# Optimization experiments

Measured on AMD Instinct MI355X. Metric: run time of the kernel, lower is better.

Reference implementation:

```python
import jax, jax.numpy as jnp
import numpy as np

NV, NA, T, FD, C, E = 192, 64, 128, 1024, 128, 262144
SPK = 3
N = (NV + NA) * T  # 32768 total graph nodes
NEG = -1e30


def _seg_max(msg, dst, mask):
    # masked scatter-max; PyG fills segments with no messages with 0
    m = jnp.where(mask[:, None], msg, NEG)
    out = jax.ops.segment_max(m, dst, num_segments=N)
    return jnp.where(out > NEG * 0.5, out, 0.0)


def _edge_conv(x, src, dst, mask, W1, b1, W2, b2):
    # EdgeConv: max_j MLP(cat[x_i, x_j - x_i])
    xi = x[dst]
    h = jnp.concatenate([xi, x[src] - xi], axis=-1)  # [E, 2C]
    h = jax.nn.relu(h @ W1 + b1) @ W2 + b2
    return _seg_max(h, dst, mask)


def _sage_conv(x, src, dst, mask, Wl, bl, Wr):
    # SAGEConv: lin_l(mean_j x_j) + lin_r(x_i), lin_r has no bias
    mf = mask.astype(x.dtype)
    s = jax.ops.segment_sum(x[src] * mf[:, None], dst, num_segments=N)
    cnt = jax.ops.segment_sum(mf, dst, num_segments=N)
    mean = s / jnp.maximum(cnt, 1.0)[:, None]
    return mean @ Wl + bl + x @ Wr


def setup_inputs():
    ks = jax.random.split(jax.random.key(0), 24)
    s = 0.05
    vals = jnp.array([-3, -2, -1, 0, 1, 3], jnp.int32)
    return {
        "x_visual": jax.random.normal(ks[0], (NV, T, FD), jnp.float32),
        "x_audio": jax.random.normal(ks[1], (NA, T, FD), jnp.float32),
        "W011": jax.random.normal(ks[2], (FD, C)) * s, "b011": jnp.zeros((C,)),
        "W012": jax.random.normal(ks[3], (FD, C)) * s, "b012": jnp.zeros((C,)),
        "ecA_W1": jax.random.normal(ks[4], (2 * C, C)) * s, "ecA_b1": jnp.zeros((C,)),
        "ecA_W2": jax.random.normal(ks[5], (C, C)) * s, "ecA_b2": jnp.zeros((C,)),
        "ec1_W1": jax.random.normal(ks[6], (2 * C, C)) * s, "ec1_b1": jnp.zeros((C,)),
        "ec1_W2": jax.random.normal(ks[7], (C, C)) * s, "ec1_b2": jnp.zeros((C,)),
        "ec2_W1": jax.random.normal(ks[8], (2 * C, C)) * s, "ec2_b1": jnp.zeros((C,)),
        "ec2_W2": jax.random.normal(ks[9], (C, C)) * s, "ec2_b2": jnp.zeros((C,)),
        "ec3_W1": jax.random.normal(ks[10], (2 * C, C)) * s, "ec3_b1": jnp.zeros((C,)),
        "ec3_W2": jax.random.normal(ks[11], (C, C)) * s, "ec3_b2": jnp.zeros((C,)),
        "sage_Wl": jax.random.normal(ks[12], (C, C)) * s, "sage_bl": jnp.zeros((C,)),
        "sage_Wr": jax.random.normal(ks[13], (C, C)) * s,
        "fc_W": jax.random.normal(ks[14], (C, 1)) * s, "fc_b": jnp.zeros((1,)),
        "edge_index": jax.random.randint(ks[15], (2, E), 0, N, dtype=jnp.int32),
        "edge_attr": vals[jax.random.randint(ks[16], (E,), 0, 6)],
        "speakers": SPK,
    }


def reference(x_visual, x_audio, W011, b011, W012, b012,
              ecA_W1, ecA_b1, ecA_W2, ecA_b2,
              ec1_W1, ec1_b1, ec1_W2, ec1_b2,
              ec2_W1, ec2_b1, ec2_W2, ec2_b2,
              ec3_W1, ec3_b1, ec3_W2, ec3_b2,
              sage_Wl, sage_bl, sage_Wr, fc_W, fc_b,
              edge_index, edge_attr, speakers):
    xv = x_visual @ W011 + b011          # [NV, T, C]
    xa = x_audio @ W012 + b012           # [NA, T, C]
    x = jnp.concatenate([xv, xa], axis=0).reshape(-1, C)  # [N, C]
    src, dst = edge_index[0], edge_index[1]
    m_audio = edge_attr == -2
    m_vpa = edge_attr == -3
    m_acv = edge_attr == 3
    m1 = (edge_attr >= 0) & (edge_attr <= 1)
    m2 = (edge_attr <= 0) & (edge_attr >= -1)
    m3 = jnp.abs(edge_attr) <= 1
    # Visual_Add_Audio_GNN: max-aggregate (x_i + x_j)
    xa_g = jax.nn.relu(_seg_max(x[dst] + x[src], dst, m_vpa))
    a = jax.nn.relu(_edge_conv(xa_g, src, dst, m_audio, ecA_W1, ecA_b1, ecA_W2, ecA_b2))
    a_res = a @ fc_W + fc_b              # [N, 1] per-node audio scores
    # Audio_Weight_Add_Visual_GNN: sum-aggregate (w_j * x_j + x_i)
    wmsg = jnp.where(m_acv[:, None], a_res[src] * x[src] + x[dst], 0.0)
    xv2 = jax.nn.relu(jax.ops.segment_sum(wmsg, dst, num_segments=N))

    def branch(mask, W1, b1, W2, b2):
        h = jax.nn.relu(_edge_conv(xv2, src, dst, mask, W1, b1, W2, b2))
        return jax.nn.relu(_sage_conv(h, src, dst, mask, sage_Wl, sage_bl, sage_Wr))

    xo = (branch(m1, ec1_W1, ec1_b1, ec1_W2, ec1_b2)
          + branch(m2, ec2_W1, ec2_b1, ec2_W2, ec2_b2)
          + branch(m3, ec3_W1, ec3_b1, ec3_W2, ec3_b2))
    # gather main-speaker visual nodes
    idx = (jnp.arange(0, NV * T, speakers * T)[:, None] + jnp.arange(T)).reshape(-1)
    return xo[idx]
```

## Files before the change

kernel.cpp:

```cpp
#include <hip/hip_runtime.h>
#include <cstdint>
#include <cstddef>

#define NVv 192
#define NAa 64
#define TT 128
#define FDd 1024
#define CCc 128
#define EEe 262144
#define NNn 32768

typedef _Float16 f16x8 __attribute__((ext_vector_type(8)));
typedef float f32x4 __attribute__((ext_vector_type(4)));

#define CAP0 65536
#define CAP1 65536
#define CAP2 65536
#define CAP3 98304
#define CAP4 98304
#define CAP5 147456
#define ARENA_TOTAL (CAP0+CAP1+CAP2+CAP3+CAP4+CAP5)

__device__ __forceinline__ void eval_masks(int a, bool m[6]) {
    m[0] = (a == -3); m[1] = (a == -2); m[2] = (a == 3);
    m[3] = (a >= 0) & (a <= 1);
    m[4] = (a >= -1) & (a <= 0);
    m[5] = (a >= -1) & (a <= 1);
}

__global__ __launch_bounds__(256) void k_zero(float* __restrict__ p) {
    size_t i = (size_t)blockIdx.x * 1024 + (size_t)threadIdx.x * 4;
    *(float4*)(p + i) = make_float4(0.f, 0.f, 0.f, 0.f);
}

__global__ __launch_bounds__(256) void k_zero4(
    const int* __restrict__ hist, const int* __restrict__ base,
    float* __restrict__ AH0, float* __restrict__ AH1,
    float* __restrict__ AH2, float* __restrict__ AH3)
{
    int col = threadIdx.x & 127, sub = threadIdx.x >> 7;
    const int js[4] = {1, 3, 4, 5};
    float* AHs[4] = {AH0, AH1, AH2, AH3};
    for (int d = blockIdx.x * 2 + sub; d < NNn; d += gridDim.x * 2) {
#pragma unroll
        for (int jj = 0; jj < 4; ++jj) {
            int j = js[jj];
            int c = hist[j * NNn + d];
            bool need;
            if (c == 0) need = true;
            else {
                int b = base[j * NNn + d], e = b + c;
                need = ((b & 63) == 0) || ((e & 63) == 0) || ((b >> 6) != ((e - 1) >> 6));
            }
            if (need) AHs[jj][(size_t)d * 128 + col] = 0.f;
        }
    }
}

__global__ __launch_bounds__(256) void k_wprep_big(
    const float* __restrict__ W011, const float* __restrict__ W012,
    _Float16* __restrict__ dst)
{
    int idx = blockIdx.x * 256 + threadIdx.x;
    int which = idx >> 17;
    int r = idx & 131071;
    int n = r >> 10, k = r & 1023;
    const float* src = which ? W012 : W011;
    dst[idx] = (_Float16)src[k * 128 + n];
}

struct WSmall { const float* p[14]; };

__global__ __launch_bounds__(256) void k_wprep_small(WSmall ws, _Float16* __restrict__ dst)
{
    int idx = blockIdx.x * 256 + threadIdx.x;
    int seg = idx >> 14;
    int r = idx & 16383;
    int n = r >> 7, k = r & 127;
    const float* src = ws.p[seg];
    float v = src[k * 128 + n];
    if (seg < 12 && (seg % 3) == 0) v -= src[16384 + k * 128 + n];
    dst[idx] = (_Float16)v;
}

__global__ __launch_bounds__(256) void k_hist(
    const int* __restrict__ attr, const int* __restrict__ edst,
    int* __restrict__ hist)
{
    int e = blockIdx.x * 256 + threadIdx.x;
    int a = attr[e], d = edst[e];
    bool m[6]; eval_masks(a, m);
#pragma unroll
    for (int j = 0; j < 6; ++j)
        if (m[j]) atomicAdd(&hist[j * NNn + d], 1);
}

__global__ __launch_bounds__(256) void k_scan_a(
    const int* __restrict__ hist, int* __restrict__ base, int* __restrict__ bsum)
{
    __shared__ int wsum[4];
    int bid = blockIdx.x;
    int idx = bid * 256 + threadIdx.x;
    int tid = threadIdx.x, lane = tid & 63, wv = tid >> 6;
    int v = hist[idx];
    int x = v;
#pragma unroll
    for (int off = 1; off < 64; off <<= 1) {
        int y = __shfl_up(x, off, 64);
        if (lane >= off) x += y;
    }
    if (lane == 63) wsum[wv] = x;
    __syncthreads();
    int add = 0;
    for (int w = 0; w < wv; ++w) add += wsum[w];
    base[idx] = add + x - v;
    if (tid == 255) bsum[bid] = add + x;
}

__global__ __launch_bounds__(384) void k_scan_b(int* __restrict__ bsum, int* __restrict__ cnts)
{
    int wv = threadIdx.x >> 6;
    int lane = threadIdx.x & 63;
    int run = 0;
#pragma unroll
    for (int c0 = 0; c0 < 128; c0 += 64) {
        int v = bsum[wv * 128 + c0 + lane];
        int x = v;
#pragma unroll
        for (int off = 1; off < 64; off <<= 1) {
            int y = __shfl_up(x, off, 64);
            if (lane >= off) x += y;
        }
        bsum[wv * 128 + c0 + lane] = run + (x - v);
        run += __shfl(x, 63, 64);
    }
    if (lane == 0) cnts[wv] = run;
}

__global__ __launch_bounds__(256) void k_scan_c(int* __restrict__ base, const int* __restrict__ bsum)
{
    base[blockIdx.x * 256 + threadIdx.x] += bsum[blockIdx.x];
}

__global__ __launch_bounds__(256) void k_fill(
    const int* __restrict__ esrc, const int* __restrict__ edst,
    const int* __restrict__ attr, const int* __restrict__ base,
    int* __restrict__ fill, int2* __restrict__ arena)
{
    int e = blockIdx.x * 256 + threadIdx.x;
    int a = attr[e];
    int s = esrc[e], d = edst[e];
    bool m[6]; eval_masks(a, m);
    const int caps[6] = {CAP0, CAP1, CAP2, CAP3, CAP4, CAP5};
    const int offs[6] = {0, CAP0, CAP0+CAP1, CAP0+CAP1+CAP2,
                         CAP0+CAP1+CAP2+CAP3, CAP0+CAP1+CAP2+CAP3+CAP4};
#pragma unroll
    for (int j = 0; j < 6; ++j) {
        if (m[j]) {
            int pos = base[j * NNn + d] + atomicAdd(&fill[j * NNn + d], 1);
            if (pos < caps[j]) arena[offs[j] + pos] = make_int2(s, d);
        }
    }
}

__global__ __launch_bounds__(512) void k_proj(
    const float* __restrict__ xv, const float* __restrict__ xa,
    const _Float16* __restrict__ BTv, const _Float16* __restrict__ BTa,
    float* __restrict__ Pp0, float* __restrict__ Pp1)
{
    __shared__ _Float16 Bl[2][128][136];
    const int tid = threadIdx.x, wave = tid >> 6, lane = tid & 63;
    const int tile = blockIdx.x >> 1, kh = blockIdx.x & 1;
    const float* A; const _Float16* BT; int mbase, obase;
    if (tile < 192) { A = xv; BT = BTv; mbase = tile * 128; obase = mbase; }
    else { A = xa; BT = BTa; mbase = (tile - 192) * 128; obase = 24576 + mbase; }
    float* Pout = kh ? Pp1 : Pp0;
    const int kbase = kh * 512;

    const int mrow = mbase + wave * 16 + (lane & 15);
    const int fk   = (lane >> 4) * 8;
    f32x4 acc[8];
#pragma unroll
    for (int i = 0; i < 8; ++i) acc[i] = (f32x4){0,0,0,0};

#pragma unroll
    for (int it = 0; it < 4; ++it) {
        int c = it * 512 + tid;
        int n = c >> 4, koff = (c & 15) * 8;
        *(f16x8*)&Bl[0][n][koff] = *(const f16x8*)(BT + (size_t)n * 1024 + kbase + koff);
    }
    f16x8 af[4];
#pragma unroll
    for (int t4 = 0; t4 < 4; ++t4) {
        const float* asrc = A + (size_t)mrow * 1024 + kbase + t4 * 32 + fk;
        float4 a0 = *(const float4*)asrc;
        float4 a1 = *(const float4*)(asrc + 4);
        af[t4] = (f16x8){ (_Float16)a0.x, (_Float16)a0.y, (_Float16)a0.z, (_Float16)a0.w,
                          (_Float16)a1.x, (_Float16)a1.y, (_Float16)a1.z, (_Float16)a1.w };
    }
    __syncthreads();

    for (int kc = 0; kc < 4; ++kc) {
        const int cur = kc & 1;
        f16x8 nf[4];
        if (kc < 3) {
            const int nxt = cur ^ 1;
#pragma unroll
            for (int it = 0; it < 4; ++it) {
                int c = it * 512 + tid;
                int n = c >> 4, koff = (c & 15) * 8;
                *(f16x8*)&Bl[nxt][n][koff] =
                    *(const f16x8*)(BT + (size_t)n * 1024 + kbase + (kc + 1) * 128 + koff);
            }
#pragma unroll
            for (int t4 = 0; t4 < 4; ++t4) {
                const float* asrc = A + (size_t)mrow * 1024 + kbase + (kc + 1) * 128 + t4 * 32 + fk;
                float4 a0 = *(const float4*)asrc;
                float4 a1 = *(const float4*)(asrc + 4);
                nf[t4] = (f16x8){ (_Float16)a0.x, (_Float16)a0.y, (_Float16)a0.z, (_Float16)a0.w,
                                  (_Float16)a1.x, (_Float16)a1.y, (_Float16)a1.z, (_Float16)a1.w };
            }
        }
#pragma unroll
        for (int t4 = 0; t4 < 4; ++t4)
#pragma unroll
            for (int nt = 0; nt < 8; ++nt) {
                f16x8 bf = *(const f16x8*)&Bl[cur][nt * 16 + (lane & 15)][t4 * 32 + fk];
                acc[nt] = __builtin_amdgcn_mfma_f32_16x16x32_f16(af[t4], bf, acc[nt], 0, 0, 0);
            }
        if (kc < 3) {
#pragma unroll
            for (int t4 = 0; t4 < 4; ++t4) af[t4] = nf[t4];
        }
        __syncthreads();
    }
    const int cbase = lane & 15, rloc = (lane >> 4) * 4;
    const int wgrp = wave & 3;
    float* Hsf = (float*)&Bl[0][0][0] + (size_t)wgrp * 16 * 132;
#pragma unroll
    for (int grp = 0; grp < 2; ++grp) {
        if ((wave >> 2) == grp) {
#pragma unroll
            for (int nt = 0; nt < 8; ++nt) {
                int c2 = nt * 16 + cbase;
#pragma unroll
                for (int rr = 0; rr < 4; ++rr)
                    Hsf[(rloc + rr) * 132 + c2] = acc[nt][rr];
            }
#pragma unroll
            for (int it = 0; it < 8; ++it) {
                int id = it * 64 + lane;
                int row = id >> 5, off = (id & 31) * 4;
                float4 v = *(float4*)&Hsf[row * 132 + off];
                *(float4*)&Pout[(size_t)(obase + wave * 16 + row) * 128 + off] = v;
            }
        }
        __syncthreads();
    }
}

__global__ __launch_bounds__(256) void k_reduce(
    const float* __restrict__ Pp0, const float* __restrict__ Pp1,
    const float* __restrict__ b011, const float* __restrict__ b012,
    float* __restrict__ X)
{
    size_t f = (size_t)blockIdx.x * 256 + threadIdx.x;
    size_t i = f * 4;
    int col = (int)(i & 127);
    int row = (int)(i >> 7);
    const float* bias = (row < 24576) ? b011 : b012;
    float4 a = *(const float4*)(Pp0 + i);
    float4 b = *(const float4*)(Pp1 + i);
    float4 bb = *(const float4*)(bias + col);
    float4 o = make_float4(a.x + b.x + bb.x, a.y + b.y + bb.y,
                           a.z + b.z + bb.z, a.w + b.w + bb.w);
    *(float4*)(X + i) = o;
}

__global__ __launch_bounds__(256) void k_pv(
    const float* __restrict__ A,
    const _Float16* __restrict__ BT1, const float* __restrict__ b1,
    const _Float16* __restrict__ BT2,
    _Float16* __restrict__ P, _Float16* __restrict__ V)
{
    __shared__ _Float16 Bl1[128][136];
    __shared__ _Float16 Bl2[128][136];
    __shared__ float bb[128];
    const int tid = threadIdx.x, wave = tid >> 6, lane = tid & 63;
    const int r0 = blockIdx.x * 64 + wave * 16;

    const int fk = (lane >> 4) * 8;
    const int mrow = blockIdx.x * 64 + wave * 16 + (lane & 15);
    float4 a0[4], a1[4];
#pragma unroll
    for (int t4 = 0; t4 < 4; ++t4) {
        const float* asrc = A + (size_t)mrow * 128 + t4 * 32 + fk;
        a0[t4] = *(const float4*)asrc;
        a1[t4] = *(const float4*)(asrc + 4);
    }
#pragma unroll
    for (int it = 0; it < 8; ++it) {
        int c = it * 256 + tid;
        int n = c >> 4, koff = (c & 15) * 8;
        *(f16x8*)&Bl1[n][koff] = *(const f16x8*)(BT1 + (size_t)n * 128 + koff);
        *(f16x8*)&Bl2[n][koff] = *(const f16x8*)(BT2 + (size_t)n * 128 + koff);
    }
    if (tid < 128) bb[tid] = b1[tid];
    __syncthreads();

    f16x8 af[4];
#pragma unroll
    for (int t4 = 0; t4 < 4; ++t4)
        af[t4] = (f16x8){ (_Float16)a0[t4].x, (_Float16)a0[t4].y, (_Float16)a0[t4].z, (_Float16)a0[t4].w,
                          (_Float16)a1[t4].x, (_Float16)a1[t4].y, (_Float16)a1[t4].z, (_Float16)a1[t4].w };
    f32x4 acc1[8], acc2[8];
#pragma unroll
    for (int i = 0; i < 8; ++i) { acc1[i] = (f32x4){0,0,0,0}; acc2[i] = (f32x4){0,0,0,0}; }
#pragma unroll
    for (int t4 = 0; t4 < 4; ++t4)
#pragma unroll
        for (int nt = 0; nt < 8; ++nt) {
            f16x8 bf1 = *(const f16x8*)&Bl1[nt * 16 + (lane & 15)][t4 * 32 + fk];
            f16x8 bf2 = *(const f16x8*)&Bl2[nt * 16 + (lane & 15)][t4 * 32 + fk];
            acc1[nt] = __builtin_amdgcn_mfma_f32_16x16x32_f16(af[t4], bf1, acc1[nt], 0, 0, 0);
            acc2[nt] = __builtin_amdgcn_mfma_f32_16x16x32_f16(af[t4], bf2, acc2[nt], 0, 0, 0);
        }
    __syncthreads();
    _Float16* Hs = &Bl1[0][0] + (size_t)wave * 16 * 136;
    const int cbase = lane & 15, rloc = (lane >> 4) * 4;
#pragma unroll
    for (int nt = 0; nt < 8; ++nt) {
        int c2 = nt * 16 + cbase;
        float bvv = bb[c2];
#pragma unroll
        for (int rr = 0; rr < 4; ++rr)
            Hs[(rloc + rr) * 136 + c2] = (_Float16)(acc1[nt][rr] + bvv);
    }
#pragma unroll
    for (int it = 0; it < 4; ++it) {
        int id = it * 64 + lane;
        int row = id >> 4, koff = (id & 15) * 8;
        *(f16x8*)&P[(size_t)(r0 + row) * 128 + koff] = *(f16x8*)&Hs[row * 136 + koff];
    }
#pragma unroll
    for (int nt = 0; nt < 8; ++nt) {
        int c2 = nt * 16 + cbase;
#pragma unroll
        for (int rr = 0; rr < 4; ++rr)
            Hs[(rloc + rr) * 136 + c2] = (_Float16)acc2[nt][rr];
    }
#pragma unroll
    for (int it = 0; it < 4; ++it) {
        int id = it * 64 + lane;
        int row = id >> 4, koff = (id & 15) * 8;
        *(f16x8*)&V[(size_t)(r0 + row) * 128 + koff] = *(f16x8*)&Hs[row * 136 + koff];
    }
}

__global__ __launch_bounds__(256, 3) void k_edge_mlp(
    const _Float16* __restrict__ P, const _Float16* __restrict__ V,
    const _Float16* __restrict__ W2T, const float* __restrict__ b2,
    const int2* __restrict__ list, const int* __restrict__ cntp, int cap,
    float* __restrict__ agg)
{
    __shared__ _Float16 Rl[64][136];
    __shared__ _Float16 W2l[128][136];
    __shared__ float b2l[128];
    __shared__ int2 eSD[64];
    __shared__ unsigned char gstart[66];
    __shared__ int gdst[64];
    __shared__ int ngrS;

    int cnt = min(*cntp, cap);
    int ntiles = (cnt + 63) >> 6;
    if ((int)blockIdx.x >= ntiles) return;

    const int tid  = threadIdx.x;
    const int wave = tid >> 6;
    const int lane = tid & 63;

#pragma unroll
    for (int i = 0; i < 8; ++i) {
        int c = tid + i * 256;
        int n = c >> 4, koff = (c & 15) * 8;
        *(f16x8*)&W2l[n][koff] = *(const f16x8*)(W2T + n * 128 + koff);
    }
    if (tid < 128) b2l[tid] = b2[tid];

    const int col   = tid & 127;
    const int half  = tid >> 7;
    const int frow  = wave * 16 + (lane & 15);
    const int fq    = (lane >> 4) * 8;
    const int rbase = wave * 16 + (lane >> 4) * 4;
    const int cbase = lane & 15;
    const int rrow  = tid >> 4;
    const int rch   = (tid & 15) * 8;

    for (int t = blockIdx.x; t < ntiles; t += gridDim.x) {
        __syncthreads();
        if (tid < 64) {
            int e = t * 64 + tid;
            eSD[tid] = (e < cnt) ? list[e] : make_int2(0, -1);
        }
        __syncthreads();
        if (tid < 64) {
            int d = eSD[tid].y;
            bool flag = (tid == 0) || (d != eSD[tid - 1].y);
            unsigned long long bm = __ballot(flag);
            int rank = (int)__popcll(bm & ((1ull << tid) - 1ull));
            if (flag) { gstart[rank] = (unsigned char)tid; gdst[rank] = d; }
            if (tid == 0) {
                int ng = (int)__popcll(bm);
                ngrS = ng;
                gstart[ng] = 64;
            }
        }
#pragma unroll
        for (int p = 0; p < 4; ++p) {
            int i = p * 16 + rrow;
            int2 sd = eSD[i];
            f16x8 rv = {0, 0, 0, 0, 0, 0, 0, 0};
            if (sd.y >= 0) {
                f16x8 pv = *(const f16x8*)(P + (size_t)sd.y * 128 + rch);
                f16x8 vv = *(const f16x8*)(V + (size_t)sd.x * 128 + rch);
                rv = pv + vv;
#pragma unroll
                for (int q = 0; q < 8; ++q)
                    rv[q] = (rv[q] > (_Float16)0.f) ? rv[q] : (_Float16)0.f;
            }
            *(f16x8*)&Rl[i][rch] = rv;
        }
        __syncthreads();

        f32x4 acc[8];
#pragma unroll
        for (int i = 0; i < 8; ++i) acc[i] = (f32x4){0,0,0,0};
#pragma unroll
        for (int t4 = 0; t4 < 4; ++t4) {
            f16x8 af = *(const f16x8*)&Rl[frow][t4 * 32 + fq];
#pragma unroll
            for (int nt = 0; nt < 8; ++nt) {
                f16x8 bf = *(const f16x8*)&W2l[nt * 16 + (lane & 15)][t4 * 32 + fq];
                acc[nt] = __builtin_amdgcn_mfma_f32_16x16x32_f16(af, bf, acc[nt], 0, 0, 0);
            }
        }
        __syncthreads();
#pragma unroll
        for (int nt = 0; nt < 8; ++nt) {
            int c2 = nt * 16 + cbase;
            float bv = b2l[c2];
#pragma unroll
            for (int rr = 0; rr < 4; ++rr)
                Rl[rbase + rr][c2] = (_Float16)fmaxf(acc[nt][rr] + bv, 0.f);
        }
        __syncthreads();
        int ng = ngrS;
        for (int g = half; g < ng; g += 2) {
            int s = gstart[g], e = gstart[g + 1];
            int d = gdst[g];
            if (d < 0) continue;
            float m = 0.f;
            for (int i = s; i < e; ++i)
                m = fmaxf(m, (float)Rl[i][col]);
            size_t o = (size_t)d * 128 + col;
            if (s == 0 || e == 64)
                atomicMax((unsigned int*)&agg[o], __float_as_uint(m));
            else
                agg[o] = m;
        }
    }
}

__global__ __launch_bounds__(256) void k_csr_vpa(
    const float* __restrict__ X, const int2* __restrict__ list,
    const int* __restrict__ base, const int* __restrict__ cntarr, int cap,
    float* __restrict__ S)
{
    int col = threadIdx.x & 127;
    int sub = threadIdx.x >> 7;
    for (int d = blockIdx.x * 2 + sub; d < NNn; d += gridDim.x * 2) {
        int c = cntarr[d];
        float v = 0.f;
        if (c > 0) {
            int b = base[d];
            int end = min(b + c, cap);
            float mx = -3.0e38f;
            for (int i = b; i < end; ++i)
                mx = fmaxf(mx, X[(size_t)list[i].x * 128 + col]);
            v = fmaxf(X[(size_t)d * 128 + col] + mx, 0.f);
        }
        S[(size_t)d * 128 + col] = v;
    }
}

__global__ __launch_bounds__(256) void k_csr_acv(
    const float* __restrict__ X, const float* __restrict__ ares,
    const int2* __restrict__ list,
    const int* __restrict__ base, const int* __restrict__ cntarr, int cap,
    float* __restrict__ S)
{
    int col = threadIdx.x & 127;
    int sub = threadIdx.x >> 7;
    for (int d = blockIdx.x * 2 + sub; d < NNn; d += gridDim.x * 2) {
        int c = cntarr[d];
        float v = 0.f;
        if (c > 0) {
            int b = base[d];
            int end = min(b + c, cap);
            float s = 0.f;
            for (int i = b; i < end; ++i) {
                int sr = list[i].x;
                s += ares[sr] * X[(size_t)sr * 128 + col];
            }
            v = fmaxf(s + (float)c * X[(size_t)d * 128 + col], 0.f);
        }
        S[(size_t)d * 128 + col] = v;
    }
}

__global__ __launch_bounds__(256) void k_csr_meanc(
    const float* __restrict__ AH, const int2* __restrict__ list,
    const int* __restrict__ basej, const int* __restrict__ histj, int cap,
    const int* __restrict__ spk, int ntarg,
    float* __restrict__ S1c, float* __restrict__ AHc)
{
    int col = threadIdx.x & 127;
    int sub = threadIdx.x >> 7;
    int step = spk[0] * TT;
    for (int ci = blockIdx.x * 2 + sub; ci < ntarg; ci += gridDim.x * 2) {
        int d = (ci >> 7) * step + (ci & 127);
        int c = histj[d];
        float v = 0.f;
        if (c > 0) {
            int b = basej[d];
            int end = min(b + c, cap);
            float s = 0.f;
            for (int i = b; i < end; ++i)
                s += AH[(size_t)list[i].x * 128 + col];
            v = s / (float)c;
        }
        S1c[(size_t)ci * 128 + col] = v;
        AHc[(size_t)ci * 128 + col] = AH[(size_t)d * 128 + col];
    }
}

__global__ __launch_bounds__(256) void k_fc(
    const float* __restrict__ A, const float* __restrict__ W,
    const float* __restrict__ b, float* __restrict__ ares)
{
    int node = blockIdx.x * 4 + (threadIdx.x >> 6);
    int lane = threadIdx.x & 63;
    const float* row = A + (size_t)node * 128;
    float v = row[lane] * W[lane] + row[lane + 64] * W[lane + 64];
#pragma unroll
    for (int off = 32; off > 0; off >>= 1) v += __shfl_down(v, off, 64);
    if (lane == 0) ares[node] = v + b[0];
}

__global__ __launch_bounds__(256) void k_sage_out(
    const float* __restrict__ S1c, const float* __restrict__ AHc,
    const _Float16* __restrict__ WlT, const _Float16* __restrict__ WrT,
    const float* __restrict__ bl, float* __restrict__ out, int ntarg)
{
    __shared__ _Float16 Al[64][40];
    __shared__ _Float16 Bl[128][40];
    const int tid  = threadIdx.x;
    const int wave = tid >> 6;
    const int lane = tid & 63;
    const int m0   = blockIdx.x * 64;

    f32x4 accB[8], accO[8];
#pragma unroll
    for (int i = 0; i < 8; ++i) { accB[i] = (f32x4){0,0,0,0}; accO[i] = (f32x4){0,0,0,0}; }

    const int ar = tid >> 2;
    const int ak = (tid & 3) * 8;
    const int fr = wave * 16 + (lane & 15);
    const int fk = (lane >> 4) * 8;
    const int rbase = wave * 16 + (lane >> 4) * 4;
    const int cbase = lane & 15;

    for (int seg = 0; seg < 6; ++seg) {
        int b = seg >> 1, which = seg & 1;
        const float* A = (which ? AHc : S1c) + (size_t)b * ntarg * 128;
        const _Float16* BT = which ? WrT : WlT;
        for (int k0 = 0; k0 < 128; k0 += 32) {
            __syncthreads();
            const float* asrc = A + (size_t)(m0 + ar) * 128 + (k0 + ak);
            float4 a0 = *(const float4*)asrc;
            float4 a1 = *(const float4*)(asrc + 4);
            f16x8 av = { (_Float16)a0.x, (_Float16)a0.y, (_Float16)a0.z, (_Float16)a0.w,
                         (_Float16)a1.x, (_Float16)a1.y, (_Float16)a1.z, (_Float16)a1.w };
            *(f16x8*)&Al[ar][ak] = av;
#pragma unroll
            for (int i = 0; i < 2; ++i) {
                int c = tid + i * 256;
                int n = c >> 2, koff = (c & 3) * 8;
                *(f16x8*)&Bl[n][koff] = *(const f16x8*)(BT + (size_t)n * 128 + k0 + koff);
            }
            __syncthreads();
            f16x8 af = *(const f16x8*)&Al[fr][fk];
#pragma unroll
            for (int nt = 0; nt < 8; ++nt) {
                f16x8 bf = *(const f16x8*)&Bl[nt * 16 + (lane & 15)][fk];
                accB[nt] = __builtin_amdgcn_mfma_f32_16x16x32_f16(af, bf, accB[nt], 0, 0, 0);
            }
        }
        if (which) {
#pragma unroll
            for (int nt = 0; nt < 8; ++nt) {
                int col = nt * 16 + cbase;
                float bv = bl[col];
#pragma unroll
                for (int rr = 0; rr < 4; ++rr) {
                    accO[nt][rr] += fmaxf(accB[nt][rr] + bv, 0.f);
                    accB[nt][rr] = 0.f;
                }
            }
        }
    }
#pragma unroll
    for (int nt = 0; nt < 8; ++nt) {
        int col = nt * 16 + cbase;
#pragma unroll
        for (int rr = 0; rr < 4; ++rr)
            out[(size_t)(m0 + rbase + rr) * 128 + col] = accO[nt][rr];
    }
}

extern "C" void kernel_launch(void* const* d_in, const int* in_sizes, int n_in,
                              void* d_out, int out_size, void* d_ws, size_t ws_size,
                              hipStream_t stream)
{
    (void)in_sizes; (void)n_in; (void)ws_size;
    const float* xv   = (const float*)d_in[0];
    const float* xa   = (const float*)d_in[1];
    const float* W011 = (const float*)d_in[2];
    const float* b011 = (const float*)d_in[3];
    const float* W012 = (const float*)d_in[4];
    const float* b012 = (const float*)d_in[5];
    const float* ecW1[4] = {(const float*)d_in[6],  (const float*)d_in[10],
                            (const float*)d_in[14], (const float*)d_in[18]};
    const float* ecb1[4] = {(const float*)d_in[7],  (const float*)d_in[11],
                            (const float*)d_in[15], (const float*)d_in[19]};
    const float* ecW2[4] = {(const float*)d_in[8],  (const float*)d_in[12],
                            (const float*)d_in[16], (const float*)d_in[20]};
    const float* ecb2[4] = {(const float*)d_in[9],  (const float*)d_in[13],
                            (const float*)d_in[17], (const float*)d_in[21]};
    const float* sageWl = (const float*)d_in[22];
    const float* sagebl = (const float*)d_in[23];
    const float* sageWr = (const float*)d_in[24];
    const float* fcW    = (const float*)d_in[25];
    const float* fcb    = (const float*)d_in[26];
    const int*   esrc   = (const int*)d_in[27];
    const int*   edst   = esrc + EEe;
    const int*   attr   = (const int*)d_in[28];
    const int*   spk    = (const int*)d_in[29];
    float* out = (float*)d_out;
    const int ntarg = out_size >> 7;

    const size_t NC = (size_t)NNn * CCc;
    float* ws   = (float*)d_ws;
    float* X    = ws;
    float* S1   = ws + 1 * NC;
    float* XV2  = ws + 2 * NC;
    float* AHc  = ws + 3 * NC;
    float* AH0  = ws + 4 * NC;
    float* AH1  = ws + 5 * NC;
    float* AH2  = ws + 6 * NC;
    float* AH3  = ws + 7 * NC;
    _Float16* P16 = (_Float16*)(ws + 8 * NC);
    _Float16* V16 = P16 + NC;
    float* ARES = ws + 9 * NC;
    int*   cnts = (int*)(ARES + NNn);
    int*   bsum = cnts + 16;
    int*   hist = bsum + 1024;
    int*   fill = hist + 6 * NNn;
    int*   base = fill + 6 * NNn;
    int2*  arena = (int2*)(base + 6 * NNn);
    _Float16* WT = (_Float16*)(arena + ARENA_TOTAL);
    float* AHb[4] = {AH0, AH1, AH2, AH3};

    const int offs[6] = {0, CAP0, CAP0+CAP1, CAP0+CAP1+CAP2,
                         CAP0+CAP1+CAP2+CAP3, CAP0+CAP1+CAP2+CAP3+CAP4};
    const int caps[6] = {CAP0, CAP1, CAP2, CAP3, CAP4, CAP5};

    const _Float16* W011T = WT;
    const _Float16* W012T = WT + 131072;
    const _Float16* WTs   = WT + 262144;
    const _Float16* WlT   = WTs + 12 * 16384;
    const _Float16* WrT   = WTs + 13 * 16384;

    k_wprep_big<<<1024, 256, 0, stream>>>(W011, W012, WT);
    WSmall wsm;
    for (int i = 0; i < 4; ++i) {
        wsm.p[3*i + 0] = ecW1[i];
        wsm.p[3*i + 1] = ecW1[i] + 16384;
        wsm.p[3*i + 2] = ecW2[i];
    }
    wsm.p[12] = sageWl; wsm.p[13] = sageWr;
    k_wprep_small<<<896, 256, 0, stream>>>(wsm, (_Float16*)WTs);
    k_zero<<<(2 * 6 * NNn) / 1024, 256, 0, stream>>>((float*)hist);
    k_hist<<<EEe / 256, 256, 0, stream>>>(attr, edst, hist);
    k_scan_a<<<768, 256, 0, stream>>>(hist, base, bsum);
    k_scan_b<<<1, 384, 0, stream>>>(bsum, cnts);
    k_scan_c<<<768, 256, 0, stream>>>(base, bsum);
    k_fill<<<EEe / 256, 256, 0, stream>>>(esrc, edst, attr, base, fill, arena);
    k_zero4<<<2048, 256, 0, stream>>>(hist, base, AH0, AH1, AH2, AH3);

    k_proj<<<512, 512, 0, stream>>>(xv, xa, W011T, W012T, S1, XV2);
    k_reduce<<<(int)(NC / 1024), 256, 0, stream>>>(S1, XV2, b011, b012, X);
    k_csr_vpa<<<2048, 256, 0, stream>>>(X, arena + offs[0], base + 0 * NNn,
                                        hist + 0 * NNn, caps[0], S1);
    k_pv<<<512, 256, 0, stream>>>(S1, WTs, ecb1[0], WTs + 16384, P16, V16);
    k_edge_mlp<<<2048, 256, 0, stream>>>(P16, V16, WTs + 2 * 16384, ecb2[0],
                                         arena + offs[1], cnts + 1, caps[1], AH0);
    k_fc<<<NNn / 4, 256, 0, stream>>>(AH0, fcW, fcb, ARES);
    k_csr_acv<<<2048, 256, 0, stream>>>(X, ARES, arena + offs[2], base + 2 * NNn,
                                        hist + 2 * NNn, caps[2], XV2);
    for (int b = 0; b < 3; ++b) {
        int j = 3 + b;
        const _Float16* Wd = WTs + (3 * (b + 1)) * 16384;
        k_pv<<<512, 256, 0, stream>>>(XV2, Wd, ecb1[b + 1], Wd + 16384, P16, V16);
        k_edge_mlp<<<2048, 256, 0, stream>>>(P16, V16, Wd + 2 * 16384, ecb2[b + 1],
                                             arena + offs[j], cnts + j, caps[j], AHb[b + 1]);
        k_csr_meanc<<<2048, 256, 0, stream>>>(AHb[b + 1], arena + offs[j], base + j * NNn,
                                              hist + j * NNn, caps[j], spk, ntarg,
                                              S1 + (size_t)b * ntarg * 128,
                                              AHc + (size_t)b * ntarg * 128);
    }
    k_sage_out<<<ntarg / 64, 256, 0, stream>>>(S1, AHc, WlT, WrT, sagebl, out, ntarg);
}
```

Baseline: 554.4 us.

## Batch three branch passes into single launches and merge setup kernels

Merges the weight prep and histogram zeroing into one setup kernel, and the CSR fill and AH zeroing into one kernel. The three branch EdgeConv stages (P/V projection, edge MLP, mean aggregation) now each run as one launch covering all three branches. Separate P/V buffers are carved out of dead workspace regions (X, AHc) so the branches can run side by side. This cuts launch count and serial dependencies and gives the GPU more work per launch, at the cost of buffer aliasing risk and a one-tile-per-block edge MLP grid of 5376 blocks.

```diff
diff --git a/kernel.cpp b/kernel.cpp
--- a/kernel.cpp
+++ b/kernel.cpp
@@ -20,6 +20,12 @@
 #define CAP4 98304
 #define CAP5 147456
 #define ARENA_TOTAL (CAP0+CAP1+CAP2+CAP3+CAP4+CAP5)
+#define OFF0 0
+#define OFF1 CAP0
+#define OFF2 (CAP0+CAP1)
+#define OFF3 (CAP0+CAP1+CAP2)
+#define OFF4 (CAP0+CAP1+CAP2+CAP3)
+#define OFF5 (CAP0+CAP1+CAP2+CAP3+CAP4)
 
 __device__ __forceinline__ void eval_masks(int a, bool m[6]) {
     m[0] = (a == -3); m[1] = (a == -2); m[2] = (a == 3);
@@ -28,59 +34,38 @@
     m[5] = (a >= -1) & (a <= 1);
 }
 
-__global__ __launch_bounds__(256) void k_zero(float* __restrict__ p) {
-    size_t i = (size_t)blockIdx.x * 1024 + (size_t)threadIdx.x * 4;
-    *(float4*)(p + i) = make_float4(0.f, 0.f, 0.f, 0.f);
-}
-
-__global__ __launch_bounds__(256) void k_zero4(
-    const int* __restrict__ hist, const int* __restrict__ base,
-    float* __restrict__ AH0, float* __restrict__ AH1,
-    float* __restrict__ AH2, float* __restrict__ AH3)
-{
-    int col = threadIdx.x & 127, sub = threadIdx.x >> 7;
-    const int js[4] = {1, 3, 4, 5};
-    float* AHs[4] = {AH0, AH1, AH2, AH3};
-    for (int d = blockIdx.x * 2 + sub; d < NNn; d += gridDim.x * 2) {
-#pragma unroll
-        for (int jj = 0; jj < 4; ++jj) {
-            int j = js[jj];
-            int c = hist[j * NNn + d];
-            bool need;
-            if (c == 0) need = true;
-            else {
-                int b = base[j * NNn + d], e = b + c;
-                need = ((b & 63) == 0) || ((e & 63) == 0) || ((b >> 6) != ((e - 1) >> 6));
-            }
-            if (need) AHs[jj][(size_t)d * 128 + col] = 0.f;
-        }
-    }
-}
-
-__global__ __launch_bounds__(256) void k_wprep_big(
+struct WSmall { const float* p[14]; };
+struct PV3  { const _Float16* Wd[3]; const _Float16* Wv[3]; const float* b1[3];
+              _Float16* P[3]; _Float16* V[3]; };
+struct MLP3 { const _Float16* W2[3]; const float* b2[3];
+              const _Float16* P[3]; const _Float16* V[3]; float* AH[3]; };
+
+__global__ __launch_bounds__(256) void k_setup(
     const float* __restrict__ W011, const float* __restrict__ W012,
-    _Float16* __restrict__ dst)
-{
-    int idx = blockIdx.x * 256 + threadIdx.x;
-    int which = idx >> 17;
-    int r = idx & 131071;
-    int n = r >> 10, k = r & 1023;
-    const float* src = which ? W012 : W011;
-    dst[idx] = (_Float16)src[k * 128 + n];
-}
-
-struct WSmall { const float* p[14]; };
-
-__global__ __launch_bounds__(256) void k_wprep_small(WSmall ws, _Float16* __restrict__ dst)
-{
-    int idx = blockIdx.x * 256 + threadIdx.x;
-    int seg = idx >> 14;
-    int r = idx & 16383;
-    int n = r >> 7, k = r & 127;
-    const float* src = ws.p[seg];
-    float v = src[k * 128 + n];
-    if (seg < 12 && (seg % 3) == 0) v -= src[16384 + k * 128 + n];
-    dst[idx] = (_Float16)v;
+    WSmall wsm, _Float16* __restrict__ WT, _Float16* __restrict__ WTs,
+    float* __restrict__ hf)
+{
+    int blk = blockIdx.x, tid = threadIdx.x;
+    if (blk < 1024) {
+        int idx = blk * 256 + tid;
+        int which = idx >> 17;
+        int r = idx & 131071;
+        int n = r >> 10, k = r & 1023;
+        const float* src = which ? W012 : W011;
+        WT[idx] = (_Float16)src[k * 128 + n];
+    } else if (blk < 1920) {
+        int idx = (blk - 1024) * 256 + tid;
+        int seg = idx >> 14;
+        int r = idx & 16383;
+        int n = r >> 7, k = r & 127;
+        const float* src = wsm.p[seg];
+        float v = src[k * 128 + n];
+        if (seg < 12 && (seg % 3) == 0) v -= src[16384 + k * 128 + n];
+        WTs[idx] = (_Float16)v;
+    } else {
+        size_t i = (size_t)(blk - 1920) * 1024 + (size_t)tid * 4;
+        *(float4*)(hf + i) = make_float4(0.f, 0.f, 0.f, 0.f);
+    }
 }
 
 __global__ __launch_bounds__(256) void k_hist(
@@ -99,8 +84,7 @@
     const int* __restrict__ hist, int* __restrict__ base, int* __restrict__ bsum)
 {
     __shared__ int wsum[4];
-    int bid = blockIdx.x;
-    int idx = bid * 256 + threadIdx.x;
+    int idx = blockIdx.x * 256 + threadIdx.x;
     int tid = threadIdx.x, lane = tid & 63, wv = tid >> 6;
     int v = hist[idx];
     int x = v;
@@ -114,7 +98,7 @@
     int add = 0;
     for (int w = 0; w < wv; ++w) add += wsum[w];
     base[idx] = add + x - v;
-    if (tid == 255) bsum[bid] = add + x;
+    if (tid == 255) bsum[blockIdx.x] = add + x;
 }
 
 __global__ __launch_bounds__(384) void k_scan_b(int* __restrict__ bsum, int* __restrict__ cnts)
@@ -142,23 +126,46 @@
     base[blockIdx.x * 256 + threadIdx.x] += bsum[blockIdx.x];
 }
 
-__global__ __launch_bounds__(256) void k_fill(
+__global__ __launch_bounds__(256) void k_fill_zero(
     const int* __restrict__ esrc, const int* __restrict__ edst,
     const int* __restrict__ attr, const int* __restrict__ base,
-    int* __restrict__ fill, int2* __restrict__ arena)
-{
-    int e = blockIdx.x * 256 + threadIdx.x;
-    int a = attr[e];
-    int s = esrc[e], d = edst[e];
-    bool m[6]; eval_masks(a, m);
-    const int caps[6] = {CAP0, CAP1, CAP2, CAP3, CAP4, CAP5};
-    const int offs[6] = {0, CAP0, CAP0+CAP1, CAP0+CAP1+CAP2,
-                         CAP0+CAP1+CAP2+CAP3, CAP0+CAP1+CAP2+CAP3+CAP4};
-#pragma unroll
-    for (int j = 0; j < 6; ++j) {
-        if (m[j]) {
-            int pos = base[j * NNn + d] + atomicAdd(&fill[j * NNn + d], 1);
-            if (pos < caps[j]) arena[offs[j] + pos] = make_int2(s, d);
+    int* __restrict__ fill, int2* __restrict__ arena, const int* __restrict__ hist,
+    float* __restrict__ AH0, float* __restrict__ AH1,
+    float* __restrict__ AH2, float* __restrict__ AH3)
+{
+    int blk = blockIdx.x, tid = threadIdx.x;
+    if (blk < 1024) {
+        int e = blk * 256 + tid;
+        int a = attr[e];
+        int s = esrc[e], d = edst[e];
+        bool m[6]; eval_masks(a, m);
+        const int caps[6] = {CAP0, CAP1, CAP2, CAP3, CAP4, CAP5};
+        const int offs[6] = {OFF0, OFF1, OFF2, OFF3, OFF4, OFF5};
+#pragma unroll
+        for (int j = 0; j < 6; ++j) {
+            if (m[j]) {
+                int pos = base[j * NNn + d] + atomicAdd(&fill[j * NNn + d], 1);
+                if (pos < caps[j]) arena[offs[j] + pos] = make_int2(s, d);
+            }
+        }
+    } else {
+        int zb = blk - 1024;
+        int col = tid & 127, sub = tid >> 7;
+        const int js[4] = {1, 3, 4, 5};
+        float* AHs[4] = {AH0, AH1, AH2, AH3};
+        for (int d = zb * 2 + sub; d < NNn; d += 2048 * 2) {
+#pragma unroll
+            for (int jj = 0; jj < 4; ++jj) {
+                int j = js[jj];
+                int c = hist[j * NNn + d];
+                bool need;
+                if (c == 0) need = true;
+                else {
+                    int b = base[j * NNn + d], e = b + c;
+                    need = ((b & 63) == 0) || ((e & 63) == 0) || ((b >> 6) != ((e - 1) >> 6));
+                }
+                if (need) AHs[jj][(size_t)d * 128 + col] = 0.f;
+            }
         }
     }
 }
@@ -272,25 +279,20 @@
     float4 a = *(const float4*)(Pp0 + i);
     float4 b = *(const float4*)(Pp1 + i);
     float4 bb = *(const float4*)(bias + col);
-    float4 o = make_float4(a.x + b.x + bb.x, a.y + b.y + bb.y,
-                           a.z + b.z + bb.z, a.w + b.w + bb.w);
-    *(float4*)(X + i) = o;
-}
-
-__global__ __launch_bounds__(256) void k_pv(
-    const float* __restrict__ A,
-    const _Float16* __restrict__ BT1, const float* __restrict__ b1,
-    const _Float16* __restrict__ BT2,
-    _Float16* __restrict__ P, _Float16* __restrict__ V)
-{
-    __shared__ _Float16 Bl1[128][136];
-    __shared__ _Float16 Bl2[128][136];
-    __shared__ float bb[128];
+    *(float4*)(X + i) = make_float4(a.x + b.x + bb.x, a.y + b.y + bb.y,
+                                    a.z + b.z + bb.z, a.w + b.w + bb.w);
+}
+
+__device__ __forceinline__ void pv_body(
+    const float* __restrict__ A, const _Float16* __restrict__ BT1,
+    const float* __restrict__ b1, const _Float16* __restrict__ BT2,
+    _Float16* __restrict__ P, _Float16* __restrict__ V, int tileblk,
+    _Float16 (*Bl1)[136], _Float16 (*Bl2)[136], float* bb)
+{
     const int tid = threadIdx.x, wave = tid >> 6, lane = tid & 63;
-    const int r0 = blockIdx.x * 64 + wave * 16;
-
+    const int r0 = tileblk * 64 + wave * 16;
     const int fk = (lane >> 4) * 8;
-    const int mrow = blockIdx.x * 64 + wave * 16 + (lane & 15);
+    const int mrow = r0 + (lane & 15);
     float4 a0[4], a1[4];
 #pragma unroll
     for (int t4 = 0; t4 < 4; ++t4) {
@@ -354,6 +356,123 @@
         int id = it * 64 + lane;
         int row = id >> 4, koff = (id & 15) * 8;
         *(f16x8*)&V[(size_t)(r0 + row) * 128 + koff] = *(f16x8*)&Hs[row * 136 + koff];
+    }
+}
+
+__global__ __launch_bounds__(256) void k_pv(
+    const float* __restrict__ A, const _Float16* __restrict__ BT1,
+    const float* __restrict__ b1, const _Float16* __restrict__ BT2,
+    _Float16* __restrict__ P, _Float16* __restrict__ V)
+{
+    __shared__ _Float16 Bl1[128][136];
+    __shared__ _Float16 Bl2[128][136];
+    __shared__ float bb[128];
+    pv_body(A, BT1, b1, BT2, P, V, blockIdx.x, Bl1, Bl2, bb);
+}
+
+__global__ __launch_bounds__(256) void k_pv3(const float* __restrict__ A, PV3 p)
+{
+    __shared__ _Float16 Bl1[128][136];
+    __shared__ _Float16 Bl2[128][136];
+    __shared__ float bb[128];
+    int b = blockIdx.x >> 9, t = blockIdx.x & 511;
+    pv_body(A, p.Wd[b], p.b1[b], p.Wv[b], p.P[b], p.V[b], t, Bl1, Bl2, bb);
+}
+
+__device__ __forceinline__ void mlp_tile(
+    const _Float16* __restrict__ P, const _Float16* __restrict__ V,
+    const _Float16* __restrict__ W2T, const float* __restrict__ b2,
+    const int2* __restrict__ list, int cnt, int t, float* __restrict__ agg,
+    _Float16 (*Rl)[136], _Float16 (*W2l)[136], float* b2l,
+    int2* eSD, unsigned char* gstart, int* gdst, int* ngrS)
+{
+    const int tid  = threadIdx.x;
+    const int wave = tid >> 6;
+    const int lane = tid & 63;
+#pragma unroll
+    for (int i = 0; i < 8; ++i) {
+        int c = tid + i * 256;
+        int n = c >> 4, koff = (c & 15) * 8;
+        *(f16x8*)&W2l[n][koff] = *(const f16x8*)(W2T + n * 128 + koff);
+    }
+    if (tid < 128) b2l[tid] = b2[tid];
+    if (tid < 64) {
+        int e = t * 64 + tid;
+        eSD[tid] = (e < cnt) ? list[e] : make_int2(0, -1);
+    }
+    __syncthreads();
+    if (tid < 64) {
+        int d = eSD[tid].y;
+        bool flag = (tid == 0) || (d != eSD[tid - 1].y);
+        unsigned long long bm = __ballot(flag);
+        int rank = (int)__popcll(bm & ((1ull << tid) - 1ull));
+        if (flag) { gstart[rank] = (unsigned char)tid; gdst[rank] = d; }
+        if (tid == 0) {
+            int ng = (int)__popcll(bm);
+            *ngrS = ng;
+            gstart[ng] = 64;
+        }
+    }
+    const int rrow = tid >> 4;
+    const int rch  = (tid & 15) * 8;
+#pragma unroll
+    for (int p = 0; p < 4; ++p) {
+        int i = p * 16 + rrow;
+        int2 sd = eSD[i];
+        f16x8 rv = {0, 0, 0, 0, 0, 0, 0, 0};
+        if (sd.y >= 0) {
+            f16x8 pv = *(const f16x8*)(P + (size_t)sd.y * 128 + rch);
+            f16x8 vv = *(const f16x8*)(V + (size_t)sd.x * 128 + rch);
+            rv = pv + vv;
+#pragma unroll
+            for (int q = 0; q < 8; ++q)
+                rv[q] = (rv[q] > (_Float16)0.f) ? rv[q] : (_Float16)0.f;
+        }
+        *(f16x8*)&Rl[i][rch] = rv;
+    }
+    __syncthreads();
+
+    const int frow  = wave * 16 + (lane & 15);
+    const int fq    = (lane >> 4) * 8;
+    f32x4 acc[8];
+#pragma unroll
+    for (int i = 0; i < 8; ++i) acc[i] = (f32x4){0,0,0,0};
+#pragma unroll
+    for (int t4 = 0; t4 < 4; ++t4) {
+        f16x8 af = *(const f16x8*)&Rl[frow][t4 * 32 + fq];
+#pragma unroll
+        for (int nt = 0; nt < 8; ++nt) {
+            f16x8 bf = *(const f16x8*)&W2l[nt * 16 + (lane & 15)][t4 * 32 + fq];
+            acc[nt] = __builtin_amdgcn_mfma_f32_16x16x32_f16(af, bf, acc[nt], 0, 0, 0);
+        }
+    }
+    __syncthreads();
+    const int rbase = wave * 16 + (lane >> 4) * 4;
+    const int cbase = lane & 15;
+#pragma unroll
+    for (int nt = 0; nt < 8; ++nt) {
+        int c2 = nt * 16 + cbase;
+        float bv = b2l[c2];
+#pragma unroll
+        for (int rr = 0; rr < 4; ++rr)
+            Rl[rbase + rr][c2] = (_Float16)fmaxf(acc[nt][rr] + bv, 0.f);
+    }
+    __syncthreads();
+    const int col  = tid & 127;
+    const int half = tid >> 7;
+    int ng = *ngrS;
+    for (int g = half; g < ng; g += 2) {
+        int s = gstart[g], e = gstart[g + 1];
+        int d = gdst[g];
+        if (d < 0) continue;
+        float m = 0.f;
+        for (int i = s; i < e; ++i)
+            m = fmaxf(m, (float)Rl[i][col]);
+        size_t o = (size_t)d * 128 + col;
+        if (s == 0 || e == 64)
+            atomicMax((unsigned int*)&agg[o], __float_as_uint(m));
+        else
+            agg[o] = m;
     }
 }
 
@@ -370,105 +489,38 @@
     __shared__ unsigned char gstart[66];
     __shared__ int gdst[64];
     __shared__ int ngrS;
-
     int cnt = min(*cntp, cap);
     int ntiles = (cnt + 63) >> 6;
     if ((int)blockIdx.x >= ntiles) return;
-
-    const int tid  = threadIdx.x;
-    const int wave = tid >> 6;
-    const int lane = tid & 63;
-
-#pragma unroll
-    for (int i = 0; i < 8; ++i) {
-        int c = tid + i * 256;
-        int n = c >> 4, koff = (c & 15) * 8;
-        *(f16x8*)&W2l[n][koff] = *(const f16x8*)(W2T + n * 128 + koff);
-    }
-    if (tid < 128) b2l[tid] = b2[tid];
-
-    const int col   = tid & 127;
-    const int half  = tid >> 7;
-    const int frow  = wave * 16 + (lane & 15);
-    const int fq    = (lane >> 4) * 8;
-    const int rbase = wave * 16 + (lane >> 4) * 4;
-    const int cbase = lane & 15;
-    const int rrow  = tid >> 4;
-    const int rch   = (tid & 15) * 8;
-
     for (int t = blockIdx.x; t < ntiles; t += gridDim.x) {
-        __syncthreads();
-        if (tid < 64) {
-            int e = t * 64 + tid;
-            eSD[tid] = (e < cnt) ? list[e] : make_int2(0, -1);
-        }
-        __syncthreads();
-        if (tid < 64) {
-            int d = eSD[tid].y;
-            bool flag = (tid == 0) || (d != eSD[tid - 1].y);
-            unsigned long long bm = __ballot(flag);
-            int rank = (int)__popcll(bm & ((1ull << tid) - 1ull));
-            if (flag) { gstart[rank] = (unsigned char)tid; gdst[rank] = d; }
-            if (tid == 0) {
-                int ng = (int)__popcll(bm);
-                ngrS = ng;
-                gstart[ng] = 64;
-            }
-        }
-#pragma unroll
-        for (int p = 0; p < 4; ++p) {
-            int i = p * 16 + rrow;
-            int2 sd = eSD[i];
-            f16x8 rv = {0, 0, 0, 0, 0, 0, 0, 0};
-            if (sd.y >= 0) {
-                f16x8 pv = *(const f16x8*)(P + (size_t)sd.y * 128 + rch);
-                f16x8 vv = *(const f16x8*)(V + (size_t)sd.x * 128 + rch);
-                rv = pv + vv;
-#pragma unroll
-                for (int q = 0; q < 8; ++q)
-                    rv[q] = (rv[q] > (_Float16)0.f) ? rv[q] : (_Float16)0.f;
-            }
-            *(f16x8*)&Rl[i][rch] = rv;
-        }
-        __syncthreads();
-
-        f32x4 acc[8];
-#pragma unroll
-        for (int i = 0; i < 8; ++i) acc[i] = (f32x4){0,0,0,0};
-#pragma unroll
-        for (int t4 = 0; t4 < 4; ++t4) {
-            f16x8 af = *(const f16x8*)&Rl[frow][t4 * 32 + fq];
-#pragma unroll
-            for (int nt = 0; nt < 8; ++nt) {
-                f16x8 bf = *(const f16x8*)&W2l[nt * 16 + (lane & 15)][t4 * 32 + fq];
-                acc[nt] = __builtin_amdgcn_mfma_f32_16x16x32_f16(af, bf, acc[nt], 0, 0, 0);
-            }
-        }
-        __syncthreads();
-#pragma unroll
-        for (int nt = 0; nt < 8; ++nt) {
-            int c2 = nt * 16 + cbase;
-            float bv = b2l[c2];
-#pragma unroll
-            for (int rr = 0; rr < 4; ++rr)
-                Rl[rbase + rr][c2] = (_Float16)fmaxf(acc[nt][rr] + bv, 0.f);
-        }
-        __syncthreads();
-        int ng = ngrS;
-        for (int g = half; g < ng; g += 2) {
-            int s = gstart[g], e = gstart[g + 1];
-            int d = gdst[g];
-            if (d < 0) continue;
-            float m = 0.f;
-            for (int i = s; i < e; ++i)
-                m = fmaxf(m, (float)Rl[i][col]);
-            size_t o = (size_t)d * 128 + col;
-            if (s == 0 || e == 64)
-                atomicMax((unsigned int*)&agg[o], __float_as_uint(m));
-            else
-                agg[o] = m;
-        }
-    }
+        if (t != (int)blockIdx.x) __syncthreads();
+        mlp_tile(P, V, W2T, b2, list, cnt, t, agg,
+                 Rl, W2l, b2l, eSD, gstart, gdst, &ngrS);
+    }
+}
+
+__global__ __launch_bounds__(256, 3) void k_edge_mlp3(
+    MLP3 p, const int2* __restrict__ arena, const int* __restrict__ cnts)
+{
+    __shared__ _Float16 Rl[64][136];
+    __shared__ _Float16 W2l[128][136];
+    __shared__ float b2l[128];
+    __shared__ int2 eSD[64];
+    __shared__ unsigned char gstart[66];
+    __shared__ int gdst[64];
+    __shared__ int ngrS;
+    const int caps[3] = {CAP3, CAP4, CAP5};
+    const int offs[3] = {OFF3, OFF4, OFF5};
+    int c0 = min(cnts[3], CAP3), c1 = min(cnts[4], CAP4), c2 = min(cnts[5], CAP5);
+    int n0 = (c0 + 63) >> 6, n1 = (c1 + 63) >> 6, n2 = (c2 + 63) >> 6;
+    int t = blockIdx.x, b;
+    if (t < n0) b = 0;
+    else if (t < n0 + n1) { b = 1; t -= n0; }
+    else if (t < n0 + n1 + n2) { b = 2; t -= n0 + n1; }
+    else return;
+    int cnt = min(cnts[3 + b], caps[b]);
+    mlp_tile(p.P[b], p.V[b], p.W2[b], p.b2[b], arena + offs[b], cnt, t, p.AH[b],
+             Rl, W2l, b2l, eSD, gstart, gdst, &ngrS);
 }
 
 __global__ __launch_bounds__(256) void k_csr_vpa(
@@ -518,29 +570,39 @@
     }
 }
 
-__global__ __launch_bounds__(256) void k_csr_meanc(
-    const float* __restrict__ AH, const int2* __restrict__ list,
-    const int* __restrict__ basej, const int* __restrict__ histj, int cap,
+__global__ __launch_bounds__(256) void k_meanc3(
+    float* const AH1, float* const AH2, float* const AH3,
+    const int2* __restrict__ arena,
+    const int* __restrict__ base, const int* __restrict__ hist,
     const int* __restrict__ spk, int ntarg,
     float* __restrict__ S1c, float* __restrict__ AHc)
 {
     int col = threadIdx.x & 127;
     int sub = threadIdx.x >> 7;
     int step = spk[0] * TT;
-    for (int ci = blockIdx.x * 2 + sub; ci < ntarg; ci += gridDim.x * 2) {
+    const int caps[3] = {CAP3, CAP4, CAP5};
+    const int offs[3] = {OFF3, OFF4, OFF5};
+    const float* AHs[3] = {AH1, AH2, AH3};
+    int total = 3 * ntarg;
+    for (int ci2 = blockIdx.x * 2 + sub; ci2 < total; ci2 += gridDim.x * 2) {
+        int b = ci2 / ntarg;
+        int ci = ci2 - b * ntarg;
+        int j = 3 + b;
+        const float* AH = AHs[b];
+        const int2* list = arena + offs[b];
         int d = (ci >> 7) * step + (ci & 127);
-        int c = histj[d];
+        int c = hist[j * NNn + d];
         float v = 0.f;
         if (c > 0) {
-            int b = basej[d];
-            int end = min(b + c, cap);
+            int bs = base[j * NNn + d];
+            int end = min(bs + c, caps[b]);
             float s = 0.f;
-            for (int i = b; i < end; ++i)
+            for (int i = bs; i < end; ++i)
                 s += AH[(size_t)list[i].x * 128 + col];
             v = s / (float)c;
         }
-        S1c[(size_t)ci * 128 + col] = v;
-        AHc[(size_t)ci * 128 + col] = AH[(size_t)d * 128 + col];
+        S1c[(size_t)ci2 * 128 + col] = v;
+        AHc[(size_t)ci2 * 128 + col] = AH[(size_t)d * 128 + col];
     }
 }
 
@@ -669,8 +731,12 @@
     float* AH1  = ws + 5 * NC;
     float* AH2  = ws + 6 * NC;
     float* AH3  = ws + 7 * NC;
-    _Float16* P16 = (_Float16*)(ws + 8 * NC);
-    _Float16* V16 = P16 + NC;
+    _Float16* P0 = (_Float16*)(ws + 8 * NC);
+    _Float16* V0 = P0 + NC;
+    _Float16* P1 = (_Float16*)X;
+    _Float16* V1 = P1 + NC;
+    _Float16* P2 = (_Float16*)AHc;
+    _Float16* V2 = P2 + NC;
     float* ARES = ws + 9 * NC;
     int*   cnts = (int*)(ARES + NNn);
     int*   bsum = cnts + 16;
@@ -679,19 +745,13 @@
     int*   base = fill + 6 * NNn;
     int2*  arena = (int2*)(base + 6 * NNn);
     _Float16* WT = (_Float16*)(arena + ARENA_TOTAL);
-    float* AHb[4] = {AH0, AH1, AH2, AH3};
-
-    const int offs[6] = {0, CAP0, CAP0+CAP1, CAP0+CAP1+CAP2,
-                         CAP0+CAP1+CAP2+CAP3, CAP0+CAP1+CAP2+CAP3+CAP4};
-    const int caps[6] = {CAP0, CAP1, CAP2, CAP3, CAP4, CAP5};
 
     const _Float16* W011T = WT;
     const _Float16* W012T = WT + 131072;
-    const _Float16* WTs   = WT + 262144;
+    _Float16* WTs = WT + 262144;
     const _Float16* WlT   = WTs + 12 * 16384;
     const _Float16* WrT   = WTs + 13 * 16384;
 
-    k_wprep_big<<<1024, 256, 0, stream>>>(W011, W012, WT);
     WSmall wsm;
     for (int i = 0; i < 4; ++i) {
         wsm.p[3*i + 0] = ecW1[i];
@@ -699,35 +759,39 @@
         wsm.p[3*i + 2] = ecW2[i];
     }
     wsm.p[12] = sageWl; wsm.p[13] = sageWr;
-    k_wprep_small<<<896, 256, 0, stream>>>(wsm, (_Float16*)WTs);
-    k_zero<<<(2 * 6 * NNn) / 1024, 256, 0, stream>>>((float*)hist);
+    k_setup<<<2304, 256, 0, stream>>>(W011, W012, wsm, WT, WTs, (float*)hist);
     k_hist<<<EEe / 256, 256, 0, stream>>>(attr, edst, hist);
     k_scan_a<<<768, 256, 0, stream>>>(hist, base, bsum);
     k_scan_b<<<1, 384, 0, stream>>>(bsum, cnts);
     k_scan_c<<<768, 256, 0, stream>>>(base, bsum);
-    k_fill<<<EEe / 256, 256, 0, stream>>>(esrc, edst, attr, base, fill, arena);
-    k_zero4<<<2048, 256, 0, stream>>>(hist, base, AH0, AH1, AH2, AH3);
+    k_fill_zero<<<3072, 256, 0, stream>>>(esrc, edst, attr, base, fill, arena, hist,
+                                          AH0, AH1, AH2, AH3);
 
     k_proj<<<512, 512, 0, stream>>>(xv, xa, W011T, W012T, S1, XV2);
     k_reduce<<<(int)(NC / 1024), 256, 0, stream>>>(S1, XV2, b011, b012, X);
-    k_csr_vpa<<<2048, 256, 0, stream>>>(X, arena + offs[0], base + 0 * NNn,
-                                        hist + 0 * NNn, caps[0], S1);
-    k_pv<<<512, 256, 0, stream>>>(S1, WTs, ecb1[0], WTs + 16384, P16, V16);
-    k_edge_mlp<<<2048, 256, 0, stream>>>(P16, V16, WTs + 2 * 16384, ecb2[0],
-                                         arena + offs[1], cnts + 1, caps[1], AH0);
+    k_csr_vpa<<<2048, 256, 0, stream>>>(X, arena + OFF0, base + 0 * NNn,
+                                        hist + 0 * NNn, CAP0, S1);
+    k_pv<<<512, 256, 0, stream>>>(S1, WTs, ecb1[0], WTs + 16384, P0, V0);
+    k_edge_mlp<<<2048, 256, 0, stream>>>(P0, V0, WTs + 2 * 16384, ecb2[0],
+                                         arena + OFF1, cnts + 1, CAP1, AH0);
     k_fc<<<NNn / 4, 256, 0, stream>>>(AH0, fcW, fcb, ARES);
-    k_csr_acv<<<2048, 256, 0, stream>>>(X, ARES, arena + offs[2], base + 2 * NNn,
-                                        hist + 2 * NNn, caps[2], XV2);
+    k_csr_acv<<<2048, 256, 0, stream>>>(X, ARES, arena + OFF2, base + 2 * NNn,
+                                        hist + 2 * NNn, CAP2, XV2);
+    PV3 pv3;
+    MLP3 m3;
+    _Float16* Pb[3] = {P0, P1, P2};
+    _Float16* Vb[3] = {V0, V1, V2};
+    float* AHb[3] = {AH1, AH2, AH3};
     for (int b = 0; b < 3; ++b) {
-        int j = 3 + b;
-        const _Float16* Wd = WTs + (3 * (b + 1)) * 16384;
-        k_pv<<<512, 256, 0, stream>>>(XV2, Wd, ecb1[b + 1], Wd + 16384, P16, V16);
-        k_edge_mlp<<<2048, 256, 0, stream>>>(P16, V16, Wd + 2 * 16384, ecb2[b + 1],
-                                             arena + offs[j], cnts + j, caps[j], AHb[b + 1]);
-        k_csr_meanc<<<2048, 256, 0, stream>>>(AHb[b + 1], arena + offs[j], base + j * NNn,
-                                              hist + j * NNn, caps[j], spk, ntarg,
-                                              S1 + (size_t)b * ntarg * 128,
-                                              AHc + (size_t)b * ntarg * 128);
-    }
+        _Float16* Wd = WTs + (3 * (b + 1)) * 16384;
+        pv3.Wd[b] = Wd; pv3.Wv[b] = Wd + 16384; pv3.b1[b] = ecb1[b + 1];
+        pv3.P[b] = Pb[b]; pv3.V[b] = Vb[b];
+        m3.W2[b] = Wd + 2 * 16384; m3.b2[b] = ecb2[b + 1];
+        m3.P[b] = Pb[b]; m3.V[b] = Vb[b]; m3.AH[b] = AHb[b];
+    }
+    k_pv3<<<1536, 256, 0, stream>>>(XV2, pv3);
+    k_edge_mlp3<<<5376, 256, 0, stream>>>(m3, arena, cnts);
+    k_meanc3<<<2048, 256, 0, stream>>>(AH1, AH2, AH3, arena, base, hist,
+                                       spk, ntarg, S1, AHc);
     k_sage_out<<<ntarg / 64, 256, 0, stream>>>(S1, AHc, WlT, WrT, sagebl, out, ntarg);
 }
```

New measurement: 523.4 us. 1.06x faster.
